# Optimization experiments

Measured on AMD Instinct MI355X. Metric: run time of the kernel, lower is better.

## Reference

```python
import jax, jax.numpy as jnp
import numpy as np

LN_EPS = 1e-5

def _layernorm(x, g, b):
    mu = jnp.mean(x, axis=-1, keepdims=True)
    var = jnp.var(x, axis=-1, keepdims=True)
    return (x - mu) * jax.lax.rsqrt(var + LN_EPS) * g + b

def setup_inputs() -> dict:
    key = jax.random.key(0)
    ks = jax.random.split(key, 8)
    B, T, V, H = 32, 128, 204, 128
    s = 0.02
    x = jax.random.normal(ks[0], (B, T, V, 1), dtype=jnp.float32)
    return {
        "x": x,
        # batched per-variable GRN params
        "fc1_w": jax.random.normal(ks[1], (V, H), dtype=jnp.float32) * s,
        "fc1_b": jnp.zeros((V, H), jnp.float32),
        "fc2_w": jax.random.normal(ks[2], (V, H, H), dtype=jnp.float32) * s,
        "fc2_b": jnp.zeros((V, H), jnp.float32),
        "glu_w": jax.random.normal(ks[3], (V, 2 * H, H), dtype=jnp.float32) * s,
        "glu_b": jnp.zeros((V, 2 * H), jnp.float32),
        "skip_w": jax.random.normal(ks[4], (V, H), dtype=jnp.float32) * s,
        "skip_b": jnp.zeros((V, H), jnp.float32),
        "ln_g": jnp.ones((H,), jnp.float32),
        "ln_b": jnp.zeros((H,), jnp.float32),
        # weight GRN params (input_dim=V, hidden=H, output_dim=V; identity skip)
        "wfc1_w": jax.random.normal(ks[5], (V, H), dtype=jnp.float32) * s,
        "wfc1_b": jnp.zeros((H,), jnp.float32),
        "wfc2_w": jax.random.normal(ks[6], (H, H), dtype=jnp.float32) * s,
        "wfc2_b": jnp.zeros((H,), jnp.float32),
        "wglu_w": jax.random.normal(ks[7], (H, 2 * V), dtype=jnp.float32) * s,
        "wglu_b": jnp.zeros((2 * V,), jnp.float32),
        "wln_g": jnp.ones((V,), jnp.float32),
        "wln_b": jnp.zeros((V,), jnp.float32),
    }

def reference(x, fc1_w, fc1_b, fc2_w, fc2_b, glu_w, glu_b, skip_w, skip_b, ln_g, ln_b,
              wfc1_w, wfc1_b, wfc2_w, wfc2_b, wglu_w, wglu_b, wln_g, wln_b):
    B, T, V, D = x.shape
    H = fc1_w.shape[1]
    xs = x.reshape(B * T, V)  # (N, V) since D == 1

    # --- batched per-variable GRN (eval mode: dropout is identity) ---
    h = jax.nn.elu(xs[..., None] * fc1_w + fc1_b)              # (N, V, H)
    h = jnp.einsum('nvh,vhk->nvk', h, fc2_w) + fc2_b           # bmm over V
    glu = jnp.einsum('nvh,vgh->nvg', h, glu_w) + glu_b         # (N, V, 2H)
    fc_out, gate = glu[..., :H], glu[..., H:]
    h = fc_out * jax.nn.sigmoid(gate)
    skip = xs[..., None] * skip_w + skip_b                     # (N, V, H)
    var_out = _layernorm(skip + h, ln_g, ln_b)                 # (N, V, H)

    # --- weight GRN (input_dim = output_dim = V -> identity skip) ---
    a = jax.nn.elu(xs @ wfc1_w + wfc1_b)                       # (N, H)
    a = a @ wfc2_w + wfc2_b
    g = a @ wglu_w + wglu_b                                    # (N, 2V)
    hg = g[:, :V] * jax.nn.sigmoid(g[:, V:])
    wts = jax.nn.softmax(_layernorm(xs + hg, wln_g, wln_b), axis=-1)  # (N, V)

    out = jnp.einsum('nvh,nv->nh', var_out, wts)               # (N, H)
    return out.reshape(B, T, H), wts.reshape(B, T, V)
```

## Files before the change

### kernel.cpp

```cpp
#include <hip/hip_runtime.h>
#include <hip/hip_bf16.h>

#define NROWS 4096
#define NV    204
#define NH    128
#define NG    256

#define SLOT_B     16384
#define SMS_OFF    (3 * SLOT_B)
#define SMS_BYTES  3584
#define LN_OFF     (SMS_OFF + 2 * SMS_BYTES)
#define LDS_BYTES  (LN_OFF + 1024)

typedef __bf16 bf16x8 __attribute__((ext_vector_type(8)));
typedef float  f32x4  __attribute__((ext_vector_type(4)));

__device__ __forceinline__ float elu_f(float x)  { return x > 0.f ? x : __expf(x) - 1.f; }
__device__ __forceinline__ float sigm_f(float x) { return 1.f / (1.f + __expf(-x)); }

__device__ __forceinline__ void stage16(const void* g, void* l) {
    __builtin_amdgcn_global_load_lds((const __attribute__((address_space(1))) void*)g,
                                     (__attribute__((address_space(3))) void*)l, 16, 0, 0);
}

__device__ __forceinline__ void stage_half(const void* src, char* dst, int w, int l) {
    const char* sb = (const char*)src;
    #pragma unroll
    for (int s = 0; s < 4; ++s)
        stage16(sb + (w * 4 + s) * 1024 + l * 16, dst + (w * 4 + s) * 1024);
}

__device__ __forceinline__ void stage_smalls(const float* src, char* dst, int w, int l) {
    if (w < 3)       stage16((const char*)src + w * 1024 + l * 16, dst + w * 1024);
    else if (l < 32) stage16((const char*)src + 3072 + l * 16,     dst + 3072);
}

#define PSYNC(N) do { \
    asm volatile("s_waitcnt vmcnt(" N ")" ::: "memory"); \
    __builtin_amdgcn_s_barrier(); \
    asm volatile("" ::: "memory"); \
} while (0)

#define NB_FC2 NV
#define NB_GLU (NV * 16)
#define NB_SM  NV
#define NB_WTS (NROWS / 8)

__global__ __launch_bounds__(256) void k_setup(
    const float* __restrict__ fc2_w, __bf16* __restrict__ fc2t,
    const float* __restrict__ glu_w, __bf16* __restrict__ glu16,
    const float* __restrict__ fc1_w, const float* __restrict__ fc1_b,
    const float* __restrict__ fc2_b, const float* __restrict__ glu_b,
    const float* __restrict__ skip_w, const float* __restrict__ skip_b,
    float* __restrict__ smalls,
    const float* __restrict__ xs,
    const float* __restrict__ wfc1_w, const float* __restrict__ wfc1_b,
    const float* __restrict__ wfc2_w, const float* __restrict__ wfc2_b,
    const float* __restrict__ wglu_w, const float* __restrict__ wglu_b,
    const float* __restrict__ wln_g,  const float* __restrict__ wln_b,
    float* __restrict__ wts)
{
    __shared__ float tile[64 * 129];
    __shared__ float sx[8][NV];
    __shared__ float sa[8][NH];
    __shared__ float sg[8][2 * NV];

    const int b = blockIdx.x;
    const int t = threadIdx.x;

    if (b < NB_FC2) {
        const int v = b;
        const float* s = fc2_w + (size_t)v * (NH * NH);
        __bf16*      d = fc2t + (size_t)v * (NH * NH);
        for (int h = 0; h < 2; ++h) {
            __syncthreads();
            for (int i = t; i < 64 * 32; i += 256) {
                const int k = i >> 5, n4 = (i & 31) * 4;
                const float4 f = *(const float4*)(s + (h * 64 + k) * 128 + n4);
                tile[k * 129 + n4 + 0] = f.x;
                tile[k * 129 + n4 + 1] = f.y;
                tile[k * 129 + n4 + 2] = f.z;
                tile[k * 129 + n4 + 3] = f.w;
            }
            __syncthreads();
            for (int i = t; i < 128 * 8; i += 256) {
                const int n = i >> 3, kc = (i & 7) * 8;
                bf16x8 o;
                #pragma unroll
                for (int q = 0; q < 8; ++q) o[q] = (__bf16)tile[(kc + q) * 129 + n];
                const int ch  = h * 8 + (i & 7);
                const int chs = ch ^ (n & 15);
                *(bf16x8*)(d + n * 128 + chs * 8) = o;
            }
        }
        return;
    }

    if (b < NB_FC2 + NB_GLU) {
        const int idx = (b - NB_FC2) * 256 + t;
        const int ch = idx & 15;
        const int g  = (idx >> 4) & 255;
        const int v  = idx >> 12;
        const float* sp = glu_w + (((size_t)v * NG + g) * NH + ch * 8);
        bf16x8 o;
        #pragma unroll
        for (int q = 0; q < 8; ++q) o[q] = (__bf16)sp[q];
        const int dch = ch ^ (g & 15);
        *(bf16x8*)(glu16 + (((size_t)v * NG + g) * NH) + dch * 8) = o;
        return;
    }

    if (b < NB_FC2 + NB_GLU + NB_SM) {
        const int v = b - (NB_FC2 + NB_GLU);
        float* dst = smalls + (size_t)v * 1024;
        for (int idx = t; idx < 896; idx += 256) {
            float val;
            if      (idx < 128)  val = fc1_w[v * NH + idx];
            else if (idx < 256)  val = fc1_b[v * NH + idx - 128];
            else if (idx < 384)  val = fc2_b[v * NH + idx - 256];
            else if (idx < 640)  val = glu_b[v * NG + idx - 384];
            else if (idx < 768)  val = skip_w[v * NH + idx - 640];
            else                 val = skip_b[v * NH + idx - 768];
            dst[idx] = val;
        }
        return;
    }

    const int r0 = (b - NB_FC2 - NB_GLU - NB_SM) * 8;
    const int tr = t >> 5;
    const int tc = t & 31;

    for (int i = t; i < 8 * NV; i += 256) {
        const int r = i / NV, c = i - r * NV;
        sx[r][c] = xs[(size_t)(r0 + r) * NV + c];
    }
    __syncthreads();

    float acc1[4];
    #pragma unroll
    for (int j = 0; j < 4; ++j) acc1[j] = wfc1_b[tc + 32 * j];
    for (int v = 0; v < NV; ++v) {
        const float xv = sx[tr][v];
        #pragma unroll
        for (int j = 0; j < 4; ++j)
            acc1[j] = fmaf(xv, wfc1_w[v * NH + tc + 32 * j], acc1[j]);
    }
    #pragma unroll
    for (int j = 0; j < 4; ++j) sa[tr][tc + 32 * j] = elu_f(acc1[j]);
    __syncthreads();

    float acc2[4];
    #pragma unroll
    for (int j = 0; j < 4; ++j) acc2[j] = wfc2_b[tc + 32 * j];
    for (int h = 0; h < NH; ++h) {
        const float av = sa[tr][h];
        #pragma unroll
        for (int j = 0; j < 4; ++j)
            acc2[j] = fmaf(av, wfc2_w[h * NH + tc + 32 * j], acc2[j]);
    }
    __syncthreads();
    #pragma unroll
    for (int j = 0; j < 4; ++j) sa[tr][tc + 32 * j] = acc2[j];
    __syncthreads();

    float accg[13];
    #pragma unroll
    for (int gi = 0; gi < 12; ++gi) accg[gi] = wglu_b[tc + 32 * gi];
    accg[12] = (tc < 24) ? wglu_b[tc + 384] : 0.f;
    for (int h = 0; h < NH; ++h) {
        const float av = sa[tr][h];
        #pragma unroll
        for (int gi = 0; gi < 12; ++gi)
            accg[gi] = fmaf(av, wglu_w[h * (2 * NV) + tc + 32 * gi], accg[gi]);
        if (tc < 24) accg[12] = fmaf(av, wglu_w[h * (2 * NV) + tc + 384], accg[12]);
    }
    __syncthreads();
    #pragma unroll
    for (int gi = 0; gi < 12; ++gi) sg[tr][tc + 32 * gi] = accg[gi];
    if (tc < 24) sg[tr][tc + 384] = accg[12];
    __syncthreads();

    float tv[7];
    float s1 = 0.f, s2 = 0.f;
    #pragma unroll
    for (int ii = 0; ii < 7; ++ii) {
        const int c = tc + 32 * ii;
        float val = 0.f;
        if (c < NV) {
            const float hg = sg[tr][c] * sigm_f(sg[tr][c + NV]);
            val = sx[tr][c] + hg;
            s1 += val; s2 = fmaf(val, val, s2);
        }
        tv[ii] = val;
    }
    #pragma unroll
    for (int m = 1; m <= 16; m <<= 1) { s1 += __shfl_xor(s1, m); s2 += __shfl_xor(s2, m); }
    const float mu  = s1 * (1.f / 204.f);
    const float var = s2 * (1.f / 204.f) - mu * mu;
    const float rs  = rsqrtf(fmaxf(var, 0.f) + 1e-5f);

    float mx = -1e30f;
    #pragma unroll
    for (int ii = 0; ii < 7; ++ii) {
        const int c = tc + 32 * ii;
        if (c < NV) {
            const float y = fmaf((tv[ii] - mu) * rs, wln_g[c], wln_b[c]);
            tv[ii] = y;
            mx = fmaxf(mx, y);
        }
    }
    #pragma unroll
    for (int m = 1; m <= 16; m <<= 1) mx = fmaxf(mx, __shfl_xor(mx, m));
    float se = 0.f;
    #pragma unroll
    for (int ii = 0; ii < 7; ++ii) {
        const int c = tc + 32 * ii;
        if (c < NV) {
            const float e = __expf(tv[ii] - mx);
            tv[ii] = e;
            se += e;
        }
    }
    #pragma unroll
    for (int m = 1; m <= 16; m <<= 1) se += __shfl_xor(se, m);
    const float inv = 1.f / se;
    #pragma unroll
    for (int ii = 0; ii < 7; ++ii) {
        const int c = tc + 32 * ii;
        if (c < NV) wts[(size_t)(r0 + tr) * NV + c] = tv[ii] * inv;
    }
}

__global__ __launch_bounds__(256, 2) void k_main(
    const float*  __restrict__ xs,
    const __bf16* __restrict__ fc2t,
    const __bf16* __restrict__ glu16,
    const float*  __restrict__ smalls,
    const float*  __restrict__ ln_g,
    const float*  __restrict__ ln_b,
    const float*  __restrict__ wts,
    float*        __restrict__ out)
{
    __shared__ __align__(16) char lds[LDS_BYTES];

    const int tid = threadIdx.x;
    const int w   = tid >> 6;
    const int l   = tid & 63;
    const int l15 = l & 15;
    const int lg  = l >> 4;

    const int vg = blockIdx.x & 7;
    const int m0 = (blockIdx.x >> 3) * 64 + w * 16;
    const int nv = (NV - 1 - vg) / 8 + 1;
    const size_t rowoff = (size_t)(m0 + l15) * NV;

    char* const slot0 = lds;
    char* const slot1 = lds + SLOT_B;
    char* const slot2 = lds + 2 * SLOT_B;

    const f32x4 zero4 = {0.f, 0.f, 0.f, 0.f};
    f32x4 acc_out[8];
    #pragma unroll
    for (int j = 0; j < 8; ++j) acc_out[j] = zero4;

    const int  sh0 = l15 + ((lg & 1) << 5);
    const int  sh1 = sh0 + 16;
    const bool rlo = (lg < 2);

    const float* lnS = (const float*)(lds + LN_OFF);

    float xv, wv, xn, wn;
    {
        if (w == 0) {
            const char* p = (l < 32) ? ((const char*)ln_g + l * 16)
                                     : ((const char*)ln_b + (l - 32) * 16);
            stage16(p, lds + LN_OFF);
        }
        stage_half(fc2t + (size_t)vg * (NH * NH), slot0, w, l);
        stage_smalls(smalls + (size_t)vg * 1024, lds + SMS_OFF, w, l);
        stage_half(fc2t + (size_t)vg * (NH * NH) + 64 * NH, slot1, w, l);
        xv = xs[rowoff + vg];
        wv = wts[rowoff + vg];
    }

    for (int i = 0; i < nv; ++i) {
        const int v  = vg + 8 * i;
        const int vn = (i + 1 < nv) ? v + 8 : v;
        const float* sm = (const float*)(lds + SMS_OFF + (i & 1) * SMS_BYTES);
        const __bf16* gluv = glu16 + (size_t)v * (NG * NH);

        PSYNC("6");
        stage_half(gluv, slot2, w, l);

        bf16x8 a1[4];
        #pragma unroll
        for (int kb = 0; kb < 4; ++kb) {
            const int k0 = kb * 32 + lg * 8;
            const float4 w0 = *(const float4*)(sm + k0);
            const float4 w1 = *(const float4*)(sm + k0 + 4);
            const float4 b0 = *(const float4*)(sm + 128 + k0);
            const float4 b1 = *(const float4*)(sm + 128 + k0 + 4);
            bf16x8 af;
            af[0] = (__bf16)elu_f(fmaf(xv, w0.x, b0.x));
            af[1] = (__bf16)elu_f(fmaf(xv, w0.y, b0.y));
            af[2] = (__bf16)elu_f(fmaf(xv, w0.z, b0.z));
            af[3] = (__bf16)elu_f(fmaf(xv, w0.w, b0.w));
            af[4] = (__bf16)elu_f(fmaf(xv, w1.x, b1.x));
            af[5] = (__bf16)elu_f(fmaf(xv, w1.y, b1.y));
            af[6] = (__bf16)elu_f(fmaf(xv, w1.z, b1.z));
            af[7] = (__bf16)elu_f(fmaf(xv, w1.w, b1.w));
            a1[kb] = af;
        }

        f32x4 h2f[8];
        #pragma unroll
        for (int j = 0; j < 4; ++j) {
            f32x4 acc = zero4;
            const char* rp = slot0 + (j * 16 + l15) * 256;
            #pragma unroll
            for (int kb = 0; kb < 4; ++kb) {
                const bf16x8 wf = *(const bf16x8*)(rp + (((kb * 4 + lg) ^ l15) << 4));
                acc = __builtin_amdgcn_mfma_f32_16x16x32_bf16(wf, a1[kb], acc, 0, 0, 0);
            }
            const float4 fb = *(const float4*)(sm + 256 + j * 16 + lg * 4);
            acc[0] += fb.x; acc[1] += fb.y; acc[2] += fb.z; acc[3] += fb.w;
            h2f[j] = acc;
        }

        PSYNC("6");
        stage_half(gluv + 64 * NH, slot0, w, l);

        #pragma unroll
        for (int j = 4; j < 8; ++j) {
            f32x4 acc = zero4;
            const char* rp = slot1 + ((j - 4) * 16 + l15) * 256;
            #pragma unroll
            for (int kb = 0; kb < 4; ++kb) {
                const bf16x8 wf = *(const bf16x8*)(rp + (((kb * 4 + lg) ^ l15) << 4));
                acc = __builtin_amdgcn_mfma_f32_16x16x32_bf16(wf, a1[kb], acc, 0, 0, 0);
            }
            const float4 fb = *(const float4*)(sm + 256 + j * 16 + lg * 4);
            acc[0] += fb.x; acc[1] += fb.y; acc[2] += fb.z; acc[3] += fb.w;
            h2f[j] = acc;
        }

        bf16x8 b2[4];
        #pragma unroll
        for (int kb2 = 0; kb2 < 4; ++kb2) {
            union U { __bf16 h[4]; int i2[2]; };
            U P, Q;
            P.h[0] = (__bf16)h2f[2 * kb2 + 0][0]; P.h[1] = (__bf16)h2f[2 * kb2 + 0][1];
            P.h[2] = (__bf16)h2f[2 * kb2 + 0][2]; P.h[3] = (__bf16)h2f[2 * kb2 + 0][3];
            Q.h[0] = (__bf16)h2f[2 * kb2 + 1][0]; Q.h[1] = (__bf16)h2f[2 * kb2 + 1][1];
            Q.h[2] = (__bf16)h2f[2 * kb2 + 1][2]; Q.h[3] = (__bf16)h2f[2 * kb2 + 1][3];
            const int px0 = __shfl(P.i2[0], sh0), qx0 = __shfl(Q.i2[0], sh0);
            const int py0 = __shfl(P.i2[1], sh0), qy0 = __shfl(Q.i2[1], sh0);
            const int px1 = __shfl(P.i2[0], sh1), qx1 = __shfl(Q.i2[0], sh1);
            const int py1 = __shfl(P.i2[1], sh1), qy1 = __shfl(Q.i2[1], sh1);
            union V { int ii[4]; bf16x8 vv; } R;
            R.ii[0] = rlo ? px0 : qx0;
            R.ii[1] = rlo ? py0 : qy0;
            R.ii[2] = rlo ? px1 : qx1;
            R.ii[3] = rlo ? py1 : qy1;
            b2[kb2] = R.vv;
        }

        PSYNC("4");
        stage_half(gluv + 128 * NH, slot1, w, l);

        f32x4 fco[8];
        #pragma unroll
        for (int j = 0; j < 4; ++j) {
            f32x4 acc = zero4;
            const char* rp = slot2 + (j * 16 + l15) * 256;
            #pragma unroll
            for (int kb = 0; kb < 4; ++kb) {
                const bf16x8 wf = *(const bf16x8*)(rp + (((kb * 4 + lg) ^ l15) << 4));
                acc = __builtin_amdgcn_mfma_f32_16x16x32_bf16(wf, b2[kb], acc, 0, 0, 0);
            }
            const float4 gb = *(const float4*)(sm + 384 + j * 16 + lg * 4);
            acc[0] += gb.x; acc[1] += gb.y; acc[2] += gb.z; acc[3] += gb.w;
            fco[j] = acc;
        }

        PSYNC("4");
        stage_half(gluv + 192 * NH, slot2, w, l);

        #pragma unroll
        for (int j = 4; j < 8; ++j) {
            f32x4 acc = zero4;
            const char* rp = slot0 + ((j - 4) * 16 + l15) * 256;
            #pragma unroll
            for (int kb = 0; kb < 4; ++kb) {
                const bf16x8 wf = *(const bf16x8*)(rp + (((kb * 4 + lg) ^ l15) << 4));
                acc = __builtin_amdgcn_mfma_f32_16x16x32_bf16(wf, b2[kb], acc, 0, 0, 0);
            }
            const float4 gb = *(const float4*)(sm + 384 + j * 16 + lg * 4);
            acc[0] += gb.x; acc[1] += gb.y; acc[2] += gb.z; acc[3] += gb.w;
            fco[j] = acc;
        }

        PSYNC("4");
        stage_half(fc2t + (size_t)vn * (NH * NH), slot0, w, l);

        f32x4 sv[8];
        #pragma unroll
        for (int j = 0; j < 4; ++j) {
            f32x4 acc = zero4;
            const char* rp = slot1 + (j * 16 + l15) * 256;
            #pragma unroll
            for (int kb = 0; kb < 4; ++kb) {
                const bf16x8 wg = *(const bf16x8*)(rp + (((kb * 4 + lg) ^ l15) << 4));
                acc = __builtin_amdgcn_mfma_f32_16x16x32_bf16(wg, b2[kb], acc, 0, 0, 0);
            }
            const float4 bga = *(const float4*)(sm + 512 + j * 16 + lg * 4);
            const float4 sw4 = *(const float4*)(sm + 640 + j * 16 + lg * 4);
            const float4 sb4 = *(const float4*)(sm + 768 + j * 16 + lg * 4);
            f32x4 s;
            s[0] = fmaf(xv, sw4.x, sb4.x) + fco[j][0] * sigm_f(acc[0] + bga.x);
            s[1] = fmaf(xv, sw4.y, sb4.y) + fco[j][1] * sigm_f(acc[1] + bga.y);
            s[2] = fmaf(xv, sw4.z, sb4.z) + fco[j][2] * sigm_f(acc[2] + bga.z);
            s[3] = fmaf(xv, sw4.w, sb4.w) + fco[j][3] * sigm_f(acc[3] + bga.w);
            sv[j] = s;
        }

        PSYNC("4");
        stage_smalls(smalls + (size_t)vn * 1024,
                     lds + SMS_OFF + ((i + 1) & 1) * SMS_BYTES, w, l);
        stage_half(fc2t + (size_t)vn * (NH * NH) + 64 * NH, slot1, w, l);
        xn = xs[rowoff + vn];
        wn = wts[rowoff + vn];

        #pragma unroll
        for (int j = 4; j < 8; ++j) {
            f32x4 acc = zero4;
            const char* rp = slot2 + ((j - 4) * 16 + l15) * 256;
            #pragma unroll
            for (int kb = 0; kb < 4; ++kb) {
                const bf16x8 wg = *(const bf16x8*)(rp + (((kb * 4 + lg) ^ l15) << 4));
                acc = __builtin_amdgcn_mfma_f32_16x16x32_bf16(wg, b2[kb], acc, 0, 0, 0);
            }
            const float4 bga = *(const float4*)(sm + 512 + j * 16 + lg * 4);
            const float4 sw4 = *(const float4*)(sm + 640 + j * 16 + lg * 4);
            const float4 sb4 = *(const float4*)(sm + 768 + j * 16 + lg * 4);
            f32x4 s;
            s[0] = fmaf(xv, sw4.x, sb4.x) + fco[j][0] * sigm_f(acc[0] + bga.x);
            s[1] = fmaf(xv, sw4.y, sb4.y) + fco[j][1] * sigm_f(acc[1] + bga.y);
            s[2] = fmaf(xv, sw4.z, sb4.z) + fco[j][2] * sigm_f(acc[2] + bga.z);
            s[3] = fmaf(xv, sw4.w, sb4.w) + fco[j][3] * sigm_f(acc[3] + bga.w);
            sv[j] = s;
        }

        float t1 = 0.f, t2 = 0.f;
        #pragma unroll
        for (int j = 0; j < 8; ++j) {
            #pragma unroll
            for (int r = 0; r < 4; ++r) { t1 += sv[j][r]; t2 = fmaf(sv[j][r], sv[j][r], t2); }
        }
        t1 += __shfl_xor(t1, 16); t2 += __shfl_xor(t2, 16);
        t1 += __shfl_xor(t1, 32); t2 += __shfl_xor(t2, 32);
        const float mu  = t1 * (1.f / 128.f);
        const float var = t2 * (1.f / 128.f) - mu * mu;
        const float rsv = rsqrtf(fmaxf(var, 0.f) + 1e-5f);

        #pragma unroll
        for (int j = 0; j < 8; ++j) {
            const float4 lg4 = *(const float4*)(lnS + j * 16 + lg * 4);
            const float4 lb4 = *(const float4*)(lnS + 128 + j * 16 + lg * 4);
            const float y0 = fmaf((sv[j][0] - mu) * rsv, lg4.x, lb4.x);
            const float y1 = fmaf((sv[j][1] - mu) * rsv, lg4.y, lb4.y);
            const float y2 = fmaf((sv[j][2] - mu) * rsv, lg4.z, lb4.z);
            const float y3 = fmaf((sv[j][3] - mu) * rsv, lg4.w, lb4.w);
            acc_out[j][0] = fmaf(wv, y0, acc_out[j][0]);
            acc_out[j][1] = fmaf(wv, y1, acc_out[j][1]);
            acc_out[j][2] = fmaf(wv, y2, acc_out[j][2]);
            acc_out[j][3] = fmaf(wv, y3, acc_out[j][3]);
        }

        xv = xn; wv = wn;
    }

    asm volatile("s_waitcnt vmcnt(0)" ::: "memory");

    #pragma unroll
    for (int j = 0; j < 8; ++j) {
        #pragma unroll
        for (int r = 0; r < 4; ++r)
            atomicAdd(&out[(size_t)(m0 + l15) * NH + j * 16 + lg * 4 + r], acc_out[j][r]);
    }
}

extern "C" void kernel_launch(void* const* d_in, const int* in_sizes, int n_in,
                              void* d_out, int out_size, void* d_ws, size_t ws_size,
                              hipStream_t stream) {
    (void)in_sizes; (void)n_in; (void)out_size; (void)ws_size;

    const float* xs     = (const float*)d_in[0];
    const float* fc1_w  = (const float*)d_in[1];
    const float* fc1_b  = (const float*)d_in[2];
    const float* fc2_w  = (const float*)d_in[3];
    const float* fc2_b  = (const float*)d_in[4];
    const float* glu_w  = (const float*)d_in[5];
    const float* glu_b  = (const float*)d_in[6];
    const float* skip_w = (const float*)d_in[7];
    const float* skip_b = (const float*)d_in[8];
    const float* ln_g   = (const float*)d_in[9];
    const float* ln_b   = (const float*)d_in[10];
    const float* wfc1_w = (const float*)d_in[11];
    const float* wfc1_b = (const float*)d_in[12];
    const float* wfc2_w = (const float*)d_in[13];
    const float* wfc2_b = (const float*)d_in[14];
    const float* wglu_w = (const float*)d_in[15];
    const float* wglu_b = (const float*)d_in[16];
    const float* wln_g  = (const float*)d_in[17];
    const float* wln_b  = (const float*)d_in[18];

    float* out = (float*)d_out;
    float* wts = out + (size_t)NROWS * NH;

    __bf16* fc2t   = (__bf16*)d_ws;
    __bf16* glu16  = fc2t + (size_t)NV * NH * NH;
    float*  smalls = (float*)(glu16 + (size_t)NV * NG * NH);

    hipMemsetAsync(d_out, 0, (size_t)NROWS * NH * sizeof(float), stream);

    k_setup<<<NB_FC2 + NB_GLU + NB_SM + NB_WTS, 256, 0, stream>>>(
        fc2_w, fc2t, glu_w, glu16,
        fc1_w, fc1_b, fc2_b, glu_b, skip_w, skip_b, smalls,
        xs, wfc1_w, wfc1_b, wfc2_w, wfc2_b, wglu_w, wglu_b, wln_g, wln_b, wts);

    k_main<<<(NROWS / 64) * 8, 256, 0, stream>>>(xs, fc2t, glu16, smalls,
                                                 ln_g, ln_b, wts, out);
}
```

Measured before the change: 330.7 us.

## Retune setup kernel rows per block, vectorize GLU conversion, seed MFMA bias, add setprio

```diff
diff --git a/kernel.cpp b/kernel.cpp
--- a/kernel.cpp
+++ b/kernel.cpp
@@ -44,7 +44,7 @@
 #define NB_FC2 NV
 #define NB_GLU (NV * 16)
 #define NB_SM  NV
-#define NB_WTS (NROWS / 8)
+#define NB_WTS (NROWS / 4)
 
 __global__ __launch_bounds__(256) void k_setup(
     const float* __restrict__ fc2_w, __bf16* __restrict__ fc2t,
@@ -61,9 +61,9 @@
     float* __restrict__ wts)
 {
     __shared__ float tile[64 * 129];
-    __shared__ float sx[8][NV];
-    __shared__ float sa[8][NH];
-    __shared__ float sg[8][2 * NV];
+    __shared__ float sx[4][NV];
+    __shared__ float sa[4][NH];
+    __shared__ float sg[4][2 * NV];
 
     const int b = blockIdx.x;
     const int t = threadIdx.x;
@@ -102,9 +102,11 @@
         const int g  = (idx >> 4) & 255;
         const int v  = idx >> 12;
         const float* sp = glu_w + (((size_t)v * NG + g) * NH + ch * 8);
+        const float4 f0 = *(const float4*)(sp);
+        const float4 f1 = *(const float4*)(sp + 4);
         bf16x8 o;
-        #pragma unroll
-        for (int q = 0; q < 8; ++q) o[q] = (__bf16)sp[q];
+        o[0] = (__bf16)f0.x; o[1] = (__bf16)f0.y; o[2] = (__bf16)f0.z; o[3] = (__bf16)f0.w;
+        o[4] = (__bf16)f1.x; o[5] = (__bf16)f1.y; o[6] = (__bf16)f1.z; o[7] = (__bf16)f1.w;
         const int dch = ch ^ (g & 15);
         *(bf16x8*)(glu16 + (((size_t)v * NG + g) * NH) + dch * 8) = o;
         return;
@@ -126,65 +128,65 @@
         return;
     }
 
-    const int r0 = (b - NB_FC2 - NB_GLU - NB_SM) * 8;
-    const int tr = t >> 5;
-    const int tc = t & 31;
-
-    for (int i = t; i < 8 * NV; i += 256) {
+    const int r0 = (b - NB_FC2 - NB_GLU - NB_SM) * 4;
+    const int tr = t >> 6;
+    const int tc = t & 63;
+
+    for (int i = t; i < 4 * NV; i += 256) {
         const int r = i / NV, c = i - r * NV;
         sx[r][c] = xs[(size_t)(r0 + r) * NV + c];
     }
     __syncthreads();
 
-    float acc1[4];
-    #pragma unroll
-    for (int j = 0; j < 4; ++j) acc1[j] = wfc1_b[tc + 32 * j];
+    float acc1[2];
+    #pragma unroll
+    for (int j = 0; j < 2; ++j) acc1[j] = wfc1_b[tc + 64 * j];
     for (int v = 0; v < NV; ++v) {
         const float xv = sx[tr][v];
         #pragma unroll
-        for (int j = 0; j < 4; ++j)
-            acc1[j] = fmaf(xv, wfc1_w[v * NH + tc + 32 * j], acc1[j]);
-    }
-    #pragma unroll
-    for (int j = 0; j < 4; ++j) sa[tr][tc + 32 * j] = elu_f(acc1[j]);
+        for (int j = 0; j < 2; ++j)
+            acc1[j] = fmaf(xv, wfc1_w[v * NH + tc + 64 * j], acc1[j]);
+    }
+    #pragma unroll
+    for (int j = 0; j < 2; ++j) sa[tr][tc + 64 * j] = elu_f(acc1[j]);
     __syncthreads();
 
-    float acc2[4];
-    #pragma unroll
-    for (int j = 0; j < 4; ++j) acc2[j] = wfc2_b[tc + 32 * j];
+    float acc2[2];
+    #pragma unroll
+    for (int j = 0; j < 2; ++j) acc2[j] = wfc2_b[tc + 64 * j];
     for (int h = 0; h < NH; ++h) {
         const float av = sa[tr][h];
         #pragma unroll
-        for (int j = 0; j < 4; ++j)
-            acc2[j] = fmaf(av, wfc2_w[h * NH + tc + 32 * j], acc2[j]);
+        for (int j = 0; j < 2; ++j)
+            acc2[j] = fmaf(av, wfc2_w[h * NH + tc + 64 * j], acc2[j]);
     }
     __syncthreads();
     #pragma unroll
-    for (int j = 0; j < 4; ++j) sa[tr][tc + 32 * j] = acc2[j];
+    for (int j = 0; j < 2; ++j) sa[tr][tc + 64 * j] = acc2[j];
     __syncthreads();
 
-    float accg[13];
-    #pragma unroll
-    for (int gi = 0; gi < 12; ++gi) accg[gi] = wglu_b[tc + 32 * gi];
-    accg[12] = (tc < 24) ? wglu_b[tc + 384] : 0.f;
+    float accg[7];
+    #pragma unroll
+    for (int gi = 0; gi < 6; ++gi) accg[gi] = wglu_b[tc + 64 * gi];
+    accg[6] = (tc < 24) ? wglu_b[tc + 384] : 0.f;
     for (int h = 0; h < NH; ++h) {
         const float av = sa[tr][h];
         #pragma unroll
-        for (int gi = 0; gi < 12; ++gi)
-            accg[gi] = fmaf(av, wglu_w[h * (2 * NV) + tc + 32 * gi], accg[gi]);
-        if (tc < 24) accg[12] = fmaf(av, wglu_w[h * (2 * NV) + tc + 384], accg[12]);
+        for (int gi = 0; gi < 6; ++gi)
+            accg[gi] = fmaf(av, wglu_w[h * (2 * NV) + tc + 64 * gi], accg[gi]);
+        if (tc < 24) accg[6] = fmaf(av, wglu_w[h * (2 * NV) + tc + 384], accg[6]);
     }
     __syncthreads();
     #pragma unroll
-    for (int gi = 0; gi < 12; ++gi) sg[tr][tc + 32 * gi] = accg[gi];
-    if (tc < 24) sg[tr][tc + 384] = accg[12];
+    for (int gi = 0; gi < 6; ++gi) sg[tr][tc + 64 * gi] = accg[gi];
+    if (tc < 24) sg[tr][tc + 384] = accg[6];
     __syncthreads();
 
-    float tv[7];
+    float tv[4];
     float s1 = 0.f, s2 = 0.f;
     #pragma unroll
-    for (int ii = 0; ii < 7; ++ii) {
-        const int c = tc + 32 * ii;
+    for (int ii = 0; ii < 4; ++ii) {
+        const int c = tc + 64 * ii;
         float val = 0.f;
         if (c < NV) {
             const float hg = sg[tr][c] * sigm_f(sg[tr][c + NV]);
@@ -194,15 +196,15 @@
         tv[ii] = val;
     }
     #pragma unroll
-    for (int m = 1; m <= 16; m <<= 1) { s1 += __shfl_xor(s1, m); s2 += __shfl_xor(s2, m); }
+    for (int m = 1; m <= 32; m <<= 1) { s1 += __shfl_xor(s1, m); s2 += __shfl_xor(s2, m); }
     const float mu  = s1 * (1.f / 204.f);
     const float var = s2 * (1.f / 204.f) - mu * mu;
     const float rs  = rsqrtf(fmaxf(var, 0.f) + 1e-5f);
 
     float mx = -1e30f;
     #pragma unroll
-    for (int ii = 0; ii < 7; ++ii) {
-        const int c = tc + 32 * ii;
+    for (int ii = 0; ii < 4; ++ii) {
+        const int c = tc + 64 * ii;
         if (c < NV) {
             const float y = fmaf((tv[ii] - mu) * rs, wln_g[c], wln_b[c]);
             tv[ii] = y;
@@ -210,11 +212,11 @@
         }
     }
     #pragma unroll
-    for (int m = 1; m <= 16; m <<= 1) mx = fmaxf(mx, __shfl_xor(mx, m));
+    for (int m = 1; m <= 32; m <<= 1) mx = fmaxf(mx, __shfl_xor(mx, m));
     float se = 0.f;
     #pragma unroll
-    for (int ii = 0; ii < 7; ++ii) {
-        const int c = tc + 32 * ii;
+    for (int ii = 0; ii < 4; ++ii) {
+        const int c = tc + 64 * ii;
         if (c < NV) {
             const float e = __expf(tv[ii] - mx);
             tv[ii] = e;
@@ -222,11 +224,11 @@
         }
     }
     #pragma unroll
-    for (int m = 1; m <= 16; m <<= 1) se += __shfl_xor(se, m);
+    for (int m = 1; m <= 32; m <<= 1) se += __shfl_xor(se, m);
     const float inv = 1.f / se;
     #pragma unroll
-    for (int ii = 0; ii < 7; ++ii) {
-        const int c = tc + 32 * ii;
+    for (int ii = 0; ii < 4; ++ii) {
+        const int c = tc + 64 * ii;
         if (c < NV) wts[(size_t)(r0 + tr) * NV + c] = tv[ii] * inv;
     }
 }
@@ -313,36 +315,36 @@
         }
 
         f32x4 h2f[8];
+        __builtin_amdgcn_s_setprio(1);
         #pragma unroll
         for (int j = 0; j < 4; ++j) {
-            f32x4 acc = zero4;
+            f32x4 acc = *(const f32x4*)(sm + 256 + j * 16 + lg * 4);
             const char* rp = slot0 + (j * 16 + l15) * 256;
             #pragma unroll
             for (int kb = 0; kb < 4; ++kb) {
                 const bf16x8 wf = *(const bf16x8*)(rp + (((kb * 4 + lg) ^ l15) << 4));
                 acc = __builtin_amdgcn_mfma_f32_16x16x32_bf16(wf, a1[kb], acc, 0, 0, 0);
             }
-            const float4 fb = *(const float4*)(sm + 256 + j * 16 + lg * 4);
-            acc[0] += fb.x; acc[1] += fb.y; acc[2] += fb.z; acc[3] += fb.w;
             h2f[j] = acc;
         }
+        __builtin_amdgcn_s_setprio(0);
 
         PSYNC("6");
         stage_half(gluv + 64 * NH, slot0, w, l);
 
+        __builtin_amdgcn_s_setprio(1);
         #pragma unroll
         for (int j = 4; j < 8; ++j) {
-            f32x4 acc = zero4;
+            f32x4 acc = *(const f32x4*)(sm + 256 + j * 16 + lg * 4);
             const char* rp = slot1 + ((j - 4) * 16 + l15) * 256;
             #pragma unroll
             for (int kb = 0; kb < 4; ++kb) {
                 const bf16x8 wf = *(const bf16x8*)(rp + (((kb * 4 + lg) ^ l15) << 4));
                 acc = __builtin_amdgcn_mfma_f32_16x16x32_bf16(wf, a1[kb], acc, 0, 0, 0);
             }
-            const float4 fb = *(const float4*)(sm + 256 + j * 16 + lg * 4);
-            acc[0] += fb.x; acc[1] += fb.y; acc[2] += fb.z; acc[3] += fb.w;
             h2f[j] = acc;
         }
+        __builtin_amdgcn_s_setprio(0);
 
         bf16x8 b2[4];
         #pragma unroll
@@ -369,60 +371,63 @@
         stage_half(gluv + 128 * NH, slot1, w, l);
 
         f32x4 fco[8];
+        __builtin_amdgcn_s_setprio(1);
         #pragma unroll
         for (int j = 0; j < 4; ++j) {
-            f32x4 acc = zero4;
+            f32x4 acc = *(const f32x4*)(sm + 384 + j * 16 + lg * 4);
             const char* rp = slot2 + (j * 16 + l15) * 256;
             #pragma unroll
             for (int kb = 0; kb < 4; ++kb) {
                 const bf16x8 wf = *(const bf16x8*)(rp + (((kb * 4 + lg) ^ l15) << 4));
                 acc = __builtin_amdgcn_mfma_f32_16x16x32_bf16(wf, b2[kb], acc, 0, 0, 0);
             }
-            const float4 gb = *(const float4*)(sm + 384 + j * 16 + lg * 4);
-            acc[0] += gb.x; acc[1] += gb.y; acc[2] += gb.z; acc[3] += gb.w;
             fco[j] = acc;
         }
+        __builtin_amdgcn_s_setprio(0);
 
         PSYNC("4");
         stage_half(gluv + 192 * NH, slot2, w, l);
 
+        __builtin_amdgcn_s_setprio(1);
         #pragma unroll
         for (int j = 4; j < 8; ++j) {
-            f32x4 acc = zero4;
+            f32x4 acc = *(const f32x4*)(sm + 384 + j * 16 + lg * 4);
             const char* rp = slot0 + ((j - 4) * 16 + l15) * 256;
             #pragma unroll
             for (int kb = 0; kb < 4; ++kb) {
                 const bf16x8 wf = *(const bf16x8*)(rp + (((kb * 4 + lg) ^ l15) << 4));
                 acc = __builtin_amdgcn_mfma_f32_16x16x32_bf16(wf, b2[kb], acc, 0, 0, 0);
             }
-            const float4 gb = *(const float4*)(sm + 384 + j * 16 + lg * 4);
-            acc[0] += gb.x; acc[1] += gb.y; acc[2] += gb.z; acc[3] += gb.w;
             fco[j] = acc;
         }
+        __builtin_amdgcn_s_setprio(0);
 
         PSYNC("4");
         stage_half(fc2t + (size_t)vn * (NH * NH), slot0, w, l);
 
         f32x4 sv[8];
+        __builtin_amdgcn_s_setprio(1);
         #pragma unroll
         for (int j = 0; j < 4; ++j) {
-            f32x4 acc = zero4;
+            f32x4 acc = *(const f32x4*)(sm + 512 + j * 16 + lg * 4);
             const char* rp = slot1 + (j * 16 + l15) * 256;
             #pragma unroll
             for (int kb = 0; kb < 4; ++kb) {
                 const bf16x8 wg = *(const bf16x8*)(rp + (((kb * 4 + lg) ^ l15) << 4));
                 acc = __builtin_amdgcn_mfma_f32_16x16x32_bf16(wg, b2[kb], acc, 0, 0, 0);
             }
-            const float4 bga = *(const float4*)(sm + 512 + j * 16 + lg * 4);
+            __builtin_amdgcn_s_setprio(0);
             const float4 sw4 = *(const float4*)(sm + 640 + j * 16 + lg * 4);
             const float4 sb4 = *(const float4*)(sm + 768 + j * 16 + lg * 4);
             f32x4 s;
-            s[0] = fmaf(xv, sw4.x, sb4.x) + fco[j][0] * sigm_f(acc[0] + bga.x);
-            s[1] = fmaf(xv, sw4.y, sb4.y) + fco[j][1] * sigm_f(acc[1] + bga.y);
-            s[2] = fmaf(xv, sw4.z, sb4.z) + fco[j][2] * sigm_f(acc[2] + bga.z);
-            s[3] = fmaf(xv, sw4.w, sb4.w) + fco[j][3] * sigm_f(acc[3] + bga.w);
+            s[0] = fmaf(xv, sw4.x, sb4.x) + fco[j][0] * sigm_f(acc[0]);
+            s[1] = fmaf(xv, sw4.y, sb4.y) + fco[j][1] * sigm_f(acc[1]);
+            s[2] = fmaf(xv, sw4.z, sb4.z) + fco[j][2] * sigm_f(acc[2]);
+            s[3] = fmaf(xv, sw4.w, sb4.w) + fco[j][3] * sigm_f(acc[3]);
             sv[j] = s;
-        }
+            __builtin_amdgcn_s_setprio(1);
+        }
+        __builtin_amdgcn_s_setprio(0);
 
         PSYNC("4");
         stage_smalls(smalls + (size_t)vn * 1024,
@@ -431,25 +436,28 @@
         xn = xs[rowoff + vn];
         wn = wts[rowoff + vn];
 
+        __builtin_amdgcn_s_setprio(1);
         #pragma unroll
         for (int j = 4; j < 8; ++j) {
-            f32x4 acc = zero4;
+            f32x4 acc = *(const f32x4*)(sm + 512 + j * 16 + lg * 4);
             const char* rp = slot2 + ((j - 4) * 16 + l15) * 256;
             #pragma unroll
             for (int kb = 0; kb < 4; ++kb) {
                 const bf16x8 wg = *(const bf16x8*)(rp + (((kb * 4 + lg) ^ l15) << 4));
                 acc = __builtin_amdgcn_mfma_f32_16x16x32_bf16(wg, b2[kb], acc, 0, 0, 0);
             }
-            const float4 bga = *(const float4*)(sm + 512 + j * 16 + lg * 4);
+            __builtin_amdgcn_s_setprio(0);
             const float4 sw4 = *(const float4*)(sm + 640 + j * 16 + lg * 4);
             const float4 sb4 = *(const float4*)(sm + 768 + j * 16 + lg * 4);
             f32x4 s;
-            s[0] = fmaf(xv, sw4.x, sb4.x) + fco[j][0] * sigm_f(acc[0] + bga.x);
-            s[1] = fmaf(xv, sw4.y, sb4.y) + fco[j][1] * sigm_f(acc[1] + bga.y);
-            s[2] = fmaf(xv, sw4.z, sb4.z) + fco[j][2] * sigm_f(acc[2] + bga.z);
-            s[3] = fmaf(xv, sw4.w, sb4.w) + fco[j][3] * sigm_f(acc[3] + bga.w);
+            s[0] = fmaf(xv, sw4.x, sb4.x) + fco[j][0] * sigm_f(acc[0]);
+            s[1] = fmaf(xv, sw4.y, sb4.y) + fco[j][1] * sigm_f(acc[1]);
+            s[2] = fmaf(xv, sw4.z, sb4.z) + fco[j][2] * sigm_f(acc[2]);
+            s[3] = fmaf(xv, sw4.w, sb4.w) + fco[j][3] * sigm_f(acc[3]);
             sv[j] = s;
-        }
+            __builtin_amdgcn_s_setprio(1);
+        }
+        __builtin_amdgcn_s_setprio(0);
 
         float t1 = 0.f, t2 = 0.f;
         #pragma unroll
```

Result: slower. 356.6 us (+7.8%).
